# Kernel optimization log

Measured on AMD Instinct MI355X. Metric: run time of the kernel, lower is better.

The kernel has to match this reference:

```python
import jax, jax.numpy as jnp
import numpy as np

N_NODES = 65536
N_EDGES = 524288
N_GRAPHS = 512
G_NODES = 10000
NUM_DISEASES = 2000
IN_DIM = 128
HID = 256  # 2 * IN_DIM (z_emb concat feat)
D_FEAT = 512
C_FEAT = 512
MAX_Z = 4000


def setup_inputs() -> dict:
    key = jax.random.key(0)
    ks = jax.random.split(key, 20)
    rn = lambda k, shape: jax.random.normal(k, shape, dtype=jnp.float32) * 0.05
    return {
        "z": jax.random.randint(ks[0], (N_NODES,), 0, MAX_Z),
        "node_id": jnp.sort(jax.random.randint(ks[1], (N_NODES,), 0, G_NODES)),
        "src": jax.random.randint(ks[2], (N_EDGES,), 0, N_NODES),
        "dst": jax.random.randint(ks[3], (N_EDGES,), 0, N_NODES),
        "graph_ids": jnp.sort(jax.random.randint(ks[4], (N_NODES,), 0, N_GRAPHS)),
        "z_table": rn(ks[5], (MAX_Z, IN_DIM)),
        "d_feat_tab": rn(ks[6], (G_NODES, D_FEAT)),
        "c_feat_tab": rn(ks[7], (G_NODES, C_FEAT)),
        "Wd": rn(ks[8], (D_FEAT, IN_DIM)),
        "Wc": rn(ks[9], (C_FEAT, IN_DIM)),
        "gin_W1": rn(ks[10], (HID, HID)), "gin_b1": jnp.zeros((HID,), jnp.float32),
        "gin_W2": rn(ks[11], (HID, HID)), "gin_b2": jnp.zeros((HID,), jnp.float32),
        "sage_Wself": rn(ks[12], (HID, HID)),
        "sage_Wneigh": rn(ks[13], (HID, HID)),
        "sage_b": jnp.zeros((HID,), jnp.float32),
        "lin1_W": rn(ks[14], (HID, HID)), "lin1_b": jnp.zeros((HID,), jnp.float32),
        "lin2_W": rn(ks[15], (HID, 1)), "lin2_b": jnp.zeros((1,), jnp.float32),
    }


def reference(z, node_id, src, dst, graph_ids, z_table, d_feat_tab, c_feat_tab,
              Wd, Wc, gin_W1, gin_b1, gin_W2, gin_b2,
              sage_Wself, sage_Wneigh, sage_b, lin1_W, lin1_b, lin2_W, lin2_b):
    # --- input feature construction (Model.forward) ---
    z_emb = z_table[z]                               # [N, IN_DIM]
    d_proj = d_feat_tab[node_id] @ Wd                # d_fc (bias=False)
    c_proj = c_feat_tab[node_id] @ Wc                # c_fc (bias=False)
    disease = (node_id <= NUM_DISEASES)[:, None]
    # node_id is sorted -> masked concat order == node order
    feat = jnp.where(disease, d_proj, c_proj)        # [N, IN_DIM]
    x = jnp.concatenate([z_emb, feat], axis=1)       # [N, HID]
    # --- GINConv: sum aggregation, eps=0, mlp = Lin->ReLU->Lin ---
    agg = jax.ops.segment_sum(x[src], dst, num_segments=N_NODES)
    h = x + agg
    h = jax.nn.relu(h @ gin_W1 + gin_b1) @ gin_W2 + gin_b2
    # --- SAGEConv('mean'): fc_self(h) + fc_neigh(mean_neighbors) + bias ---
    deg = jax.ops.segment_sum(jnp.ones((N_EDGES,), h.dtype), dst, num_segments=N_NODES)
    mean_n = jax.ops.segment_sum(h[src], dst, num_segments=N_NODES) / jnp.maximum(deg, 1.0)[:, None]
    h = h @ sage_Wself + mean_n @ sage_Wneigh + sage_b
    # --- per-graph max pooling readout ---
    g = jax.ops.segment_max(h, graph_ids, num_segments=N_GRAPHS, indices_are_sorted=True)
    g = jnp.where(jnp.isfinite(g), g, 0.0)           # guard empty graphs
    # --- head: Linear -> ReLU -> (dropout p=0, eval) -> Linear ---
    h = jax.nn.relu(g @ lin1_W + lin1_b)
    return h @ lin2_W + lin2_b                       # [N_GRAPHS, 1]
```

## Files before the change

kernel.cpp:

```cpp
#include <hip/hip_runtime.h>
#include <hip/hip_bf16.h>

#define N_NODES     65536
#define N_EDGES     524288
#define N_GRAPHS    512
#define G_NODES_N   10000
#define NUM_DIS     2000
#define IN_DIM      128
#define HID         256
#define D_FEAT      512
#define MAX_Z       4000

typedef _Float16 half8 __attribute__((ext_vector_type(8)));
typedef float    f32x4 __attribute__((ext_vector_type(4)));

typedef __attribute__((address_space(1))) const void as1_void;
typedef __attribute__((address_space(3))) void       as3_void;

__global__ __launch_bounds__(256) void prep_kernel(
    const float* __restrict__ Ws, const float* __restrict__ Wn,
    const float* __restrict__ Wd, const float* __restrict__ Wc,
    const float* __restrict__ W1, const float* __restrict__ W2,
    const float* __restrict__ z_table,
    const int* __restrict__ z, const int* __restrict__ node_id,
    _Float16* __restrict__ WsT, _Float16* __restrict__ WnT,
    _Float16* __restrict__ WdT, _Float16* __restrict__ WcT,
    _Float16* __restrict__ W12P, _Float16* __restrict__ zt16,
    int2* __restrict__ zn2, int* __restrict__ cnt, int* __restrict__ flags)
{
    const int b = blockIdx.x;
    const int tid = threadIdx.x;
    if (b < 64) {
        __shared__ float tile[64][65];
        const float* W; _Float16* T; int K, N, k0, n0;
        if (b < 32) {
            const int mat = b >> 4, t = b & 15;
            K = HID; N = HID; k0 = (t >> 2) * 64; n0 = (t & 3) * 64;
            W = (mat == 0) ? Ws : Wn;
            T = (mat == 0) ? WsT : WnT;
        } else {
            const int bb = b - 32;
            const int mat = bb >> 4, t = bb & 15;
            K = D_FEAT; N = IN_DIM; k0 = (t >> 1) * 64; n0 = (t & 1) * 64;
            W = (mat == 0) ? Wd : Wc;
            T = (mat == 0) ? WdT : WcT;
        }
        const int tx = tid & 63, ty = tid >> 6;
        #pragma unroll
        for (int r = 0; r < 64; r += 4)
            tile[r + ty][tx] = W[(size_t)(k0 + r + ty) * N + n0 + tx];
        __syncthreads();
        #pragma unroll
        for (int c = 0; c < 64; c += 4)
            T[(size_t)(n0 + c + ty) * K + k0 + tx] = (_Float16)tile[tx][c + ty];
    } else if (b < 576) {
        const int bb = b - 64;
        const int mat = bb >> 8;
        const int k = bb & 255;
        const int n = tid;
        const float* W = mat ? W2 : W1;
        const float v = W[(size_t)k * HID + n];
        const size_t idx = (size_t)(mat * 8 + (k >> 5)) * 8192
                         + (size_t)((((k >> 3) & 3) * 256 + n) * 8 + (k & 7));
        W12P[idx] = (_Float16)v;
    } else if (b < 826) {
        const size_t base = ((size_t)(b - 576) * 256 + tid) * 8;
        const float4 f0 = *(const float4*)(z_table + base);
        const float4 f1 = *(const float4*)(z_table + base + 4);
        half8 h;
        h[0]=(_Float16)f0.x; h[1]=(_Float16)f0.y; h[2]=(_Float16)f0.z; h[3]=(_Float16)f0.w;
        h[4]=(_Float16)f1.x; h[5]=(_Float16)f1.y; h[6]=(_Float16)f1.z; h[7]=(_Float16)f1.w;
        *(half8*)(zt16 + base) = h;
    } else if (b < 890) {
        const int base = (b - 826) * 1024 + tid * 4;
        *(int4*)(cnt + base) = make_int4(0, 0, 0, 0);
        if (b == 826 && tid < 128) flags[tid] = 0;
    } else {
        const int i = (b - 890) * 256 + tid;
        zn2[i] = make_int2(z[i] << 8, node_id[i] << 8);
    }
}

__global__ __launch_bounds__(256) void proj_hist_kernel(
    const float* __restrict__ dtab, const float* __restrict__ ctab,
    const _Float16* __restrict__ WdT, const _Float16* __restrict__ WcT,
    _Float16* __restrict__ proj,
    const int* __restrict__ dst, int* __restrict__ cnt)
{
    const int blk = blockIdx.x;
    if (blk >= 79) {
        const int e = (blk - 79) * 256 + threadIdx.x;
        if (e < N_EDGES) atomicAdd(&cnt[dst[e]], 1);
        return;
    }
    __shared__ _Float16 Alds[128 * 40];
    __shared__ _Float16 Blds[128 * 40];
    const float* tab; const _Float16* WT; int base, M, bm;
    if (blk < 16) { tab = dtab; WT = WdT; base = 0;           M = NUM_DIS + 1;             bm = blk * 128; }
    else          { tab = ctab; WT = WcT; base = NUM_DIS + 1; M = G_NODES_N - NUM_DIS - 1; bm = (blk - 16) * 128; }
    const int tid  = threadIdx.x;
    const int wave = tid >> 6, lane = tid & 63;
    const int q    = lane >> 4, l16 = lane & 15;
    const int mbase = (wave & 1) * 64, nbase = (wave >> 1) * 64;
    const int r = tid >> 1, s = tid & 1;

    f32x4 acc[4][4] = {};

    for (int kc = 0; kc < 16; ++kc) {
        const int k0 = kc * 32;
        const int arow = min(bm + r, M - 1);
        const float* gA = tab + (size_t)(base + arow) * D_FEAT + k0 + s * 16;
        const _Float16* gB = WT + (size_t)r * D_FEAT + k0 + s * 16;
        const float4 f0 = ((const float4*)gA)[0];
        const float4 f1 = ((const float4*)gA)[1];
        const float4 f2 = ((const float4*)gA)[2];
        const float4 f3 = ((const float4*)gA)[3];
        const half8 hb0 = *(const half8*)gB;
        const half8 hb1 = *(const half8*)(gB + 8);
        half8 h0, h1;
        h0[0]=(_Float16)f0.x; h0[1]=(_Float16)f0.y; h0[2]=(_Float16)f0.z; h0[3]=(_Float16)f0.w;
        h0[4]=(_Float16)f1.x; h0[5]=(_Float16)f1.y; h0[6]=(_Float16)f1.z; h0[7]=(_Float16)f1.w;
        h1[0]=(_Float16)f2.x; h1[1]=(_Float16)f2.y; h1[2]=(_Float16)f2.z; h1[3]=(_Float16)f2.w;
        h1[4]=(_Float16)f3.x; h1[5]=(_Float16)f3.y; h1[6]=(_Float16)f3.z; h1[7]=(_Float16)f3.w;
        __syncthreads();
        *(half8*)&Alds[r * 40 + s * 16]     = h0;
        *(half8*)&Alds[r * 40 + s * 16 + 8] = h1;
        *(half8*)&Blds[r * 40 + s * 16]     = hb0;
        *(half8*)&Blds[r * 40 + s * 16 + 8] = hb1;
        __syncthreads();
        half8 a[4], b[4];
        #pragma unroll
        for (int i = 0; i < 4; ++i)
            a[i] = *(const half8*)&Alds[(mbase + i * 16 + l16) * 40 + q * 8];
        #pragma unroll
        for (int j = 0; j < 4; ++j)
            b[j] = *(const half8*)&Blds[(nbase + j * 16 + l16) * 40 + q * 8];
        #pragma unroll
        for (int i = 0; i < 4; ++i)
            #pragma unroll
            for (int j = 0; j < 4; ++j)
                acc[i][j] = __builtin_amdgcn_mfma_f32_16x16x32_f16(a[i], b[j], acc[i][j], 0, 0, 0);
    }

    #pragma unroll
    for (int j = 0; j < 4; ++j) {
        const int colg = nbase + j * 16 + l16;
        #pragma unroll
        for (int i = 0; i < 4; ++i) {
            #pragma unroll
            for (int rr = 0; rr < 4; ++rr) {
                const int row = bm + mbase + i * 16 + q * 4 + rr;
                if (row < M)
                    proj[(size_t)(base + row) * IN_DIM + colg] = (_Float16)acc[i][j][rr];
            }
        }
    }
}

__global__ __launch_bounds__(256) void scan_fused_kernel(
    const int* __restrict__ cnt, int* __restrict__ row_ptr,
    int* __restrict__ fill, int* __restrict__ flags,
    const int2* __restrict__ zn2, int2* __restrict__ pzn,
    int2* __restrict__ prbe, int* __restrict__ pnode,
    int* __restrict__ bhist)
{
    __shared__ int a[256], b[256];
    __shared__ int sums[64];
    __shared__ int segbase;
    __shared__ int hist[64];
    __shared__ int pos[64];
    const int t = threadIdx.x;
    const int blk = blockIdx.x;
    const int base = blk * 1024 + t * 4;
    const int4 c = *(const int4*)(cnt + base);
    const int s = c.x + c.y + c.z + c.w;
    a[t] = s;
    if (t < 64) hist[t] = 0;
    __syncthreads();
    int* in = a; int* out = b;
    for (int off = 1; off < 256; off <<= 1) {
        out[t] = in[t] + ((t >= off) ? in[t - off] : 0);
        __syncthreads();
        int* tmp = in; in = out; out = tmp;
    }
    if (t == 0) {
        atomicExch(&flags[64 + blk], in[255]);
        __threadfence();
        atomicAdd(&flags[0], 1);
        while (atomicAdd(&flags[0], 0) < 64) {}
    }
    __syncthreads();
    if (t < 64) sums[t] = atomicAdd(&flags[64 + t], 0);
    __syncthreads();
    if (t == 0) {
        int pfx = 0;
        for (int i = 0; i < blk; ++i) pfx += sums[i];
        segbase = pfx;
        if (blk == 63) {
            int tot = pfx;
            for (int i = blk; i < 64; ++i) tot += sums[i];
            row_ptr[N_NODES] = tot;
        }
    }
    __syncthreads();
    const int run = in[t] - s + segbase;
    int4 r;
    r.x = run; r.y = run + c.x; r.z = r.y + c.y; r.w = r.z + c.z;
    *(int4*)(row_ptr + base) = r;
    *(int4*)(fill + base) = r;

    const int bk0 = min(c.x, 63), bk1 = min(c.y, 63);
    const int bk2 = min(c.z, 63), bk3 = min(c.w, 63);
    atomicAdd(&hist[bk0], 1); atomicAdd(&hist[bk1], 1);
    atomicAdd(&hist[bk2], 1); atomicAdd(&hist[bk3], 1);
    __syncthreads();
    if (t < 64) bhist[blk * 64 + t] = hist[t];
    __threadfence();
    if (t == 0) {
        atomicAdd(&flags[1], 1);
        while (atomicAdd(&flags[1], 0) < 64) {}
    }
    __syncthreads();
    if (t < 64) {
        int pre = 0, tot = 0;
        for (int i = 0; i < 64; ++i) {
            const int v = atomicAdd(&bhist[i * 64 + t], 0);
            if (i < blk) pre += v;
            tot += v;
        }
        hist[t] = tot;
        pos[t] = pre;
    }
    __syncthreads();
    if (t == 0) {
        int run2 = 0;
        for (int i = 0; i < 64; ++i) { const int tt = hist[i]; hist[i] = run2; run2 += tt; }
    }
    __syncthreads();
    if (t < 64) pos[t] = hist[t] + pos[t];
    __syncthreads();
    const int begs[4] = { r.x, r.y, r.z, r.w };
    const int ends[4] = { r.y, r.z, r.w, r.w + c.w };
    const int bks[4]  = { bk0, bk1, bk2, bk3 };
    #pragma unroll
    for (int k = 0; k < 4; ++k) {
        const int p = atomicAdd(&pos[bks[k]], 1);
        pzn[p]   = zn2[base + k];
        prbe[p]  = make_int2(begs[k], ends[k]);
        pnode[p] = base + k;
    }
}

__global__ __launch_bounds__(256) void scatter_kernel(
    const int* __restrict__ src, const int* __restrict__ dst,
    const int2* __restrict__ zn2,
    int* __restrict__ fill, int* __restrict__ col, int2* __restrict__ colzn)
{
    const int e = blockIdx.x * 256 + threadIdx.x;
    if (e < N_EDGES) {
        const int s = src[e];
        const int pos = atomicAdd(&fill[dst[e]], 1);
        col[pos] = s << 9;
        colzn[pos] = zn2[s];
    }
}

__global__ __launch_bounds__(256, 6) void gather_kernel(
    const int2* __restrict__ prbe, const int2* __restrict__ pzn,
    const int2* __restrict__ colzn,
    const _Float16* __restrict__ zt16, const _Float16* __restrict__ proj,
    _Float16* __restrict__ AGG)
{
    const int i = blockIdx.x * 16 + (threadIdx.x >> 4);
    const int l = threadIdx.x & 15;
    const bool isz = (l < 8);
    const char* tab = isz ? (const char*)zt16 : (const char*)proj;
    const int loff = (l & 7) * 32;
    const int2 be = prbe[i];
    const int2 zn = pzn[i];
    float acc[16];
    {
        const half8* sp = (const half8*)(tab + (isz ? zn.x : zn.y) + loff);
        const half8 v0 = sp[0], v1 = sp[1];
        #pragma unroll
        for (int k = 0; k < 8; ++k) { acc[k] = (float)v0[k]; acc[8 + k] = (float)v1[k]; }
    }
    int e = be.x;
    const int end = be.y;
    int2 iA, iB, iC, iD;
    if (e + 4 <= end) {
        iA = colzn[e]; iB = colzn[e + 1]; iC = colzn[e + 2]; iD = colzn[e + 3];
    }
    for (; e + 4 <= end; e += 4) {
        const half8* sA = (const half8*)(tab + (isz ? iA.x : iA.y) + loff);
        const half8* sB = (const half8*)(tab + (isz ? iB.x : iB.y) + loff);
        const half8* sC = (const half8*)(tab + (isz ? iC.x : iC.y) + loff);
        const half8* sD = (const half8*)(tab + (isz ? iD.x : iD.y) + loff);
        const half8 a0 = sA[0], a1 = sA[1];
        const half8 b0 = sB[0], b1 = sB[1];
        const half8 c0 = sC[0], c1 = sC[1];
        const half8 d0 = sD[0], d1 = sD[1];
        if (e + 8 <= end) {
            iA = colzn[e + 4]; iB = colzn[e + 5];
            iC = colzn[e + 6]; iD = colzn[e + 7];
        }
        #pragma unroll
        for (int k = 0; k < 8; ++k) {
            acc[k]     += ((float)a0[k] + (float)b0[k]) + ((float)c0[k] + (float)d0[k]);
            acc[8 + k] += ((float)a1[k] + (float)b1[k]) + ((float)c1[k] + (float)d1[k]);
        }
    }
    for (; e < end; ++e) {
        const int2 j = colzn[e];
        const half8* s = (const half8*)(tab + (isz ? j.x : j.y) + loff);
        const half8 v0 = s[0], v1 = s[1];
        #pragma unroll
        for (int k = 0; k < 8; ++k) { acc[k] += (float)v0[k]; acc[8 + k] += (float)v1[k]; }
    }
    half8 o0, o1;
    #pragma unroll
    for (int k = 0; k < 8; ++k) { o0[k] = (_Float16)acc[k]; o1[k] = (_Float16)acc[8 + k]; }
    _Float16* dst = AGG + (size_t)i * 256 + l * 16;
    *(half8*)dst = o0;
    *(half8*)(dst + 8) = o1;
}

__global__ __launch_bounds__(256) void gin_mlp_kernel(
    const _Float16* __restrict__ AGG, const int* __restrict__ pnode,
    const _Float16* __restrict__ W12P,
    const float* __restrict__ b1, const float* __restrict__ b2,
    _Float16* __restrict__ H)
{
    __shared__ _Float16 Apanel[64 * 264];
    __shared__ _Float16 Blds[8192];
    __shared__ int prows[64];

    const int bm   = blockIdx.x * 64;
    const int tid  = threadIdx.x;
    const int wave = tid >> 6, lane = tid & 63;
    const int q    = lane >> 4, l16 = lane & 15;
    const int nbase = wave * 64;
    const int sb   = wave * 256 + lane;

    if (tid < 64) prows[tid] = pnode[bm + tid];

    #pragma unroll
    for (int tt = 0; tt < 4; ++tt) {
        const int seg = (wave * 4 + tt) * 64 + lane;
        __builtin_amdgcn_global_load_lds((as1_void*)(W12P + seg * 8),
            (as3_void*)&Blds[(wave * 4 + tt) * 64 * 8], 16, 0, 0);
    }

    {
        const int ar = tid >> 2, acs = (tid & 3) * 64;
        const _Float16* asrc = AGG + (size_t)(bm + ar) * 256 + acs;
        half8 av[8];
        #pragma unroll
        for (int k = 0; k < 8; ++k) av[k] = *(const half8*)(asrc + k * 8);
        #pragma unroll
        for (int k = 0; k < 8; ++k)
            *(half8*)&Apanel[ar * 264 + acs + k * 8] = av[k];
    }
    __syncthreads();

    half8 pf0, pf1, pf2, pf3;
    auto pfetch = [&](int c) {
        const _Float16* s = W12P + (size_t)c * 8192 + (size_t)sb * 8;
        pf0 = *(const half8*)(s);
        pf1 = *(const half8*)(s + 512);
        pf2 = *(const half8*)(s + 1024);
        pf3 = *(const half8*)(s + 1536);
    };
    pfetch(1);

    f32x4 acc[4][4] = {};
    for (int c = 0; c < 16; ++c) {
        const int kl = (c & 7) * 32;
        half8 a[4], b[4];
        #pragma unroll
        for (int i = 0; i < 4; ++i)
            a[i] = *(const half8*)&Apanel[(i * 16 + l16) * 264 + kl + q * 8];
        #pragma unroll
        for (int j = 0; j < 4; ++j)
            b[j] = *(const half8*)&Blds[(q * 256 + nbase + j * 16 + l16) * 8];
        #pragma unroll
        for (int i = 0; i < 4; ++i)
            #pragma unroll
            for (int j = 0; j < 4; ++j)
                acc[i][j] = __builtin_amdgcn_mfma_f32_16x16x32_f16(a[i], b[j], acc[i][j], 0, 0, 0);
        if (c == 15) break;
        __syncthreads();
        *(half8*)&Blds[sb * 8]         = pf0;
        *(half8*)&Blds[(sb + 64) * 8]  = pf1;
        *(half8*)&Blds[(sb + 128) * 8] = pf2;
        *(half8*)&Blds[(sb + 192) * 8] = pf3;
        if (c == 7) {
            #pragma unroll
            for (int j = 0; j < 4; ++j) {
                const int colg = nbase + j * 16 + l16;
                const float bv = b1[colg];
                #pragma unroll
                for (int i = 0; i < 4; ++i)
                    #pragma unroll
                    for (int rr = 0; rr < 4; ++rr) {
                        const float v = fmaxf(acc[i][j][rr] + bv, 0.0f);
                        Apanel[(i * 16 + q * 4 + rr) * 264 + colg] = (_Float16)v;
                        acc[i][j][rr] = 0.0f;
                    }
            }
        }
        if (c < 14) pfetch(c + 2);
        __syncthreads();
    }

    #pragma unroll
    for (int j = 0; j < 4; ++j) {
        const int colg = nbase + j * 16 + l16;
        const float bv = b2[colg];
        #pragma unroll
        for (int i = 0; i < 4; ++i)
            #pragma unroll
            for (int rr = 0; rr < 4; ++rr) {
                const int rowl = i * 16 + q * 4 + rr;
                H[(size_t)prows[rowl] * HID + colg] = (_Float16)(acc[i][j][rr] + bv);
            }
    }
}

__global__ __launch_bounds__(256) void csr_agg_kernel(
    const int2* __restrict__ prbe, const int* __restrict__ pnode,
    const int* __restrict__ col,
    const _Float16* __restrict__ F, _Float16* __restrict__ OUT)
{
    const int t = threadIdx.x;
    const int q = t & 31;
    const int pr = t >> 5;
    const int ia = blockIdx.x * 16 + pr * 2;
    const int ib = ia + 1;
    const int2 beA = prbe[ia];
    const int2 beB = prbe[ib];
    int eA = beA.x, eB = beB.x;
    const int endA = beA.y, endB = beB.y;
    const char* Fb = (const char*)F + q * 16;
    float accA[8] = {0.f,0.f,0.f,0.f,0.f,0.f,0.f,0.f};
    float accB[8] = {0.f,0.f,0.f,0.f,0.f,0.f,0.f,0.f};

    int cA0, cA1, cA2, cA3, cB0, cB1, cB2, cB3;
    bool mA = (eA + 4 <= endA), mB = (eB + 4 <= endB);
    if (mA) { cA0 = col[eA]; cA1 = col[eA+1]; cA2 = col[eA+2]; cA3 = col[eA+3]; }
    if (mB) { cB0 = col[eB]; cB1 = col[eB+1]; cB2 = col[eB+2]; cB3 = col[eB+3]; }

    while (mA && mB) {
        const half8 a0 = *(const half8*)(Fb + cA0);
        const half8 a1 = *(const half8*)(Fb + cA1);
        const half8 a2 = *(const half8*)(Fb + cA2);
        const half8 a3 = *(const half8*)(Fb + cA3);
        const half8 b0 = *(const half8*)(Fb + cB0);
        const half8 b1 = *(const half8*)(Fb + cB1);
        const half8 b2 = *(const half8*)(Fb + cB2);
        const half8 b3 = *(const half8*)(Fb + cB3);
        eA += 4; eB += 4;
        mA = (eA + 4 <= endA); mB = (eB + 4 <= endB);
        if (mA) { cA0 = col[eA]; cA1 = col[eA+1]; cA2 = col[eA+2]; cA3 = col[eA+3]; }
        if (mB) { cB0 = col[eB]; cB1 = col[eB+1]; cB2 = col[eB+2]; cB3 = col[eB+3]; }
        #pragma unroll
        for (int k = 0; k < 8; ++k) {
            accA[k] += ((float)a0[k] + (float)a1[k]) + ((float)a2[k] + (float)a3[k]);
            accB[k] += ((float)b0[k] + (float)b1[k]) + ((float)b2[k] + (float)b3[k]);
        }
    }
    while (mA) {
        const half8 a0 = *(const half8*)(Fb + cA0);
        const half8 a1 = *(const half8*)(Fb + cA1);
        const half8 a2 = *(const half8*)(Fb + cA2);
        const half8 a3 = *(const half8*)(Fb + cA3);
        eA += 4;
        mA = (eA + 4 <= endA);
        if (mA) { cA0 = col[eA]; cA1 = col[eA+1]; cA2 = col[eA+2]; cA3 = col[eA+3]; }
        #pragma unroll
        for (int k = 0; k < 8; ++k)
            accA[k] += ((float)a0[k] + (float)a1[k]) + ((float)a2[k] + (float)a3[k]);
    }
    while (mB) {
        const half8 b0 = *(const half8*)(Fb + cB0);
        const half8 b1 = *(const half8*)(Fb + cB1);
        const half8 b2 = *(const half8*)(Fb + cB2);
        const half8 b3 = *(const half8*)(Fb + cB3);
        eB += 4;
        mB = (eB + 4 <= endB);
        if (mB) { cB0 = col[eB]; cB1 = col[eB+1]; cB2 = col[eB+2]; cB3 = col[eB+3]; }
        #pragma unroll
        for (int k = 0; k < 8; ++k)
            accB[k] += ((float)b0[k] + (float)b1[k]) + ((float)b2[k] + (float)b3[k]);
    }
    for (; eA < endA; ++eA) {
        const half8 v = *(const half8*)(Fb + col[eA]);
        #pragma unroll
        for (int k = 0; k < 8; ++k) accA[k] += (float)v[k];
    }
    for (; eB < endB; ++eB) {
        const half8 v = *(const half8*)(Fb + col[eB]);
        #pragma unroll
        for (int k = 0; k < 8; ++k) accB[k] += (float)v[k];
    }

    const float rsA = 1.0f / fmaxf((float)(endA - beA.x), 1.0f);
    const float rsB = 1.0f / fmaxf((float)(endB - beB.x), 1.0f);
    half8 oA, oB;
    #pragma unroll
    for (int k = 0; k < 8; ++k) {
        oA[k] = (_Float16)(accA[k] * rsA);
        oB[k] = (_Float16)(accB[k] * rsB);
    }
    *(half8*)(OUT + (size_t)pnode[ia] * HID + q * 8) = oA;
    *(half8*)(OUT + (size_t)pnode[ib] * HID + q * 8) = oB;
}

__global__ __launch_bounds__(256) void mfma_gemm_kernel(
    const _Float16* __restrict__ A1, const _Float16* __restrict__ A2,
    const _Float16* __restrict__ B1T, const _Float16* __restrict__ B2T,
    const float* __restrict__ bias, _Float16* __restrict__ Ch)
{
    __shared__ _Float16 Alds[128 * 32];
    __shared__ _Float16 Blds[128 * 32];
    const int bm   = blockIdx.x * 128;
    const int bn   = blockIdx.y * 128;
    const int tid  = threadIdx.x;
    const int wave = tid >> 6, lane = tid & 63;
    const int q    = lane >> 4, l16 = lane & 15;
    const int mbase = (wave & 1) * 64, nbase = (wave >> 1) * 64;

    const int i0 = wave * 128 + lane;
    const int i1 = i0 + 64;
    const int r0 = i0 >> 2, s0 = i0 & 3;
    const int r1 = i1 >> 2, s1 = i1 & 3;

    half8 pa0, pa1, pb0, pb1;
    auto pfetch = [&](int kc) {
        const int k0 = (kc & 7) * 32;
        const _Float16* Ab = (kc < 8) ? A1 : A2;
        const _Float16* Bb = (kc < 8) ? B1T : B2T;
        pa0 = *(const half8*)(Ab + (size_t)(bm + r0) * HID + k0 + s0 * 8);
        pa1 = *(const half8*)(Ab + (size_t)(bm + r1) * HID + k0 + s1 * 8);
        pb0 = *(const half8*)(Bb + (size_t)(bn + r0) * HID + k0 + s0 * 8);
        pb1 = *(const half8*)(Bb + (size_t)(bn + r1) * HID + k0 + s1 * 8);
    };
    pfetch(0);

    f32x4 acc[4][4] = {};

    for (int kc = 0; kc < 16; ++kc) {
        __syncthreads();
        *(half8*)&Alds[i0 * 8] = pa0;
        *(half8*)&Alds[i1 * 8] = pa1;
        *(half8*)&Blds[i0 * 8] = pb0;
        *(half8*)&Blds[i1 * 8] = pb1;
        if (kc < 15) pfetch(kc + 1);
        __syncthreads();
        half8 a[4], b[4];
        #pragma unroll
        for (int i = 0; i < 4; ++i)
            a[i] = *(const half8*)&Alds[(mbase + i * 16 + l16) * 32 + q * 8];
        #pragma unroll
        for (int j = 0; j < 4; ++j)
            b[j] = *(const half8*)&Blds[(nbase + j * 16 + l16) * 32 + q * 8];
        #pragma unroll
        for (int i = 0; i < 4; ++i)
            #pragma unroll
            for (int j = 0; j < 4; ++j)
                acc[i][j] = __builtin_amdgcn_mfma_f32_16x16x32_f16(a[i], b[j], acc[i][j], 0, 0, 0);
    }

    #pragma unroll
    for (int j = 0; j < 4; ++j) {
        const int colg = bn + nbase + j * 16 + l16;
        const float bv = bias[colg];
        #pragma unroll
        for (int i = 0; i < 4; ++i) {
            #pragma unroll
            for (int rr = 0; rr < 4; ++rr) {
                const int rowg = bm + mbase + i * 16 + q * 4 + rr;
                Ch[(size_t)rowg * HID + colg] = (_Float16)(acc[i][j][rr] + bv);
            }
        }
    }
}

__global__ __launch_bounds__(256) void pool_head_kernel(
    const _Float16* __restrict__ H2, const int* __restrict__ gid,
    const float* __restrict__ W1, const float* __restrict__ b1,
    const float* __restrict__ W2, const float* __restrict__ b2,
    float* __restrict__ out)
{
    const int g = blockIdx.x;
    const int tid = threadIdx.x;
    int lo = 0, hi = N_NODES;
    while (lo < hi) { const int mid = (lo + hi) >> 1; if (gid[mid] < g) lo = mid + 1; else hi = mid; }
    const int start = lo;
    hi = N_NODES;
    while (lo < hi) { const int mid = (lo + hi) >> 1; if (gid[mid] < g + 1) lo = mid + 1; else hi = mid; }
    const int end = lo;

    const int rowofs = tid >> 5;
    const int q = tid & 31;
    float m8[8];
    #pragma unroll
    for (int k = 0; k < 8; ++k) m8[k] = -INFINITY;
    for (int i = start + rowofs; i < end; i += 8) {
        const half8 v = *(const half8*)(H2 + (size_t)i * HID + q * 8);
        #pragma unroll
        for (int k = 0; k < 8; ++k) m8[k] = fmaxf(m8[k], (float)v[k]);
    }
    __shared__ float part[8][256];
    #pragma unroll
    for (int k = 0; k < 8; ++k) part[rowofs][q * 8 + k] = m8[k];
    __syncthreads();
    __shared__ float row[HID];
    __shared__ float red[HID];
    const int j = tid;
    float m = part[0][j];
    #pragma unroll
    for (int r = 1; r < 8; ++r) m = fmaxf(m, part[r][j]);
    row[j] = (m == -INFINITY) ? 0.0f : m;
    __syncthreads();
    float acc = b1[j];
    #pragma unroll 8
    for (int k = 0; k < HID; ++k)
        acc = fmaf(row[k], W1[k * HID + j], acc);
    acc = fmaxf(acc, 0.f);
    red[j] = acc * W2[j];
    __syncthreads();
    for (int s = 128; s > 0; s >>= 1) {
        if (j < s) red[j] += red[j + s];
        __syncthreads();
    }
    if (j == 0) out[g] = red[0] + b2[0];
}

extern "C" void kernel_launch(void* const* d_in, const int* in_sizes, int n_in,
                              void* d_out, int out_size, void* d_ws, size_t ws_size,
                              hipStream_t stream)
{
    const int*   z         = (const int*)d_in[0];
    const int*   node_id   = (const int*)d_in[1];
    const int*   src       = (const int*)d_in[2];
    const int*   dst       = (const int*)d_in[3];
    const int*   graph_ids = (const int*)d_in[4];
    const float* z_table   = (const float*)d_in[5];
    const float* d_feat    = (const float*)d_in[6];
    const float* c_feat    = (const float*)d_in[7];
    const float* Wd        = (const float*)d_in[8];
    const float* Wc        = (const float*)d_in[9];
    const float* gin_W1    = (const float*)d_in[10];
    const float* gin_b1    = (const float*)d_in[11];
    const float* gin_W2    = (const float*)d_in[12];
    const float* gin_b2    = (const float*)d_in[13];
    const float* sage_Wself  = (const float*)d_in[14];
    const float* sage_Wneigh = (const float*)d_in[15];
    const float* sage_b    = (const float*)d_in[16];
    const float* lin1_W    = (const float*)d_in[17];
    const float* lin1_b    = (const float*)d_in[18];
    const float* lin2_W    = (const float*)d_in[19];
    const float* lin2_b    = (const float*)d_in[20];
    float* out = (float*)d_out;

    const size_t NH = (size_t)N_NODES * HID;
    char* wsb = (char*)d_ws;
    _Float16* Hh   = (_Float16*)wsb;                     wsb += NH * 2;
    _Float16* AGGh = (_Float16*)wsb;                     wsb += NH * 2;
    _Float16* H2h  = (_Float16*)wsb;                     wsb += NH * 2;
    _Float16* AGGx = (_Float16*)wsb;                     wsb += NH * 2;
    _Float16* projh= (_Float16*)wsb;                     wsb += (size_t)G_NODES_N * IN_DIM * 2;
    _Float16* W12P = (_Float16*)wsb;                     wsb += 16 * 8192 * 2;
    _Float16* WsT  = (_Float16*)wsb;                     wsb += HID * HID * 2;
    _Float16* WnT  = (_Float16*)wsb;                     wsb += HID * HID * 2;
    _Float16* WdT  = (_Float16*)wsb;                     wsb += D_FEAT * IN_DIM * 2;
    _Float16* WcT  = (_Float16*)wsb;                     wsb += D_FEAT * IN_DIM * 2;
    _Float16* zt16 = (_Float16*)wsb;                     wsb += (size_t)MAX_Z * IN_DIM * 2;
    int2* zn2      = (int2*)wsb;                         wsb += (size_t)N_NODES * 8;
    int2* colzn    = (int2*)wsb;                         wsb += (size_t)(N_EDGES + 8) * 8;
    int2* pzn      = (int2*)wsb;                         wsb += (size_t)N_NODES * 8;
    int2* prbe     = (int2*)wsb;                         wsb += (size_t)N_NODES * 8;
    int* pnode     = (int*)wsb;                          wsb += (size_t)N_NODES * 4;
    int* bhist     = (int*)wsb;                          wsb += 64 * 64 * 4;
    int* row_ptr   = (int*)wsb;                          wsb += (N_NODES + 4) * 4;
    int* cnt       = (int*)wsb;                          wsb += N_NODES * 4;
    int* fill      = (int*)wsb;                          wsb += N_NODES * 4;
    int* col       = (int*)wsb;                          wsb += N_EDGES * 4;
    int* flags     = (int*)wsb;                          wsb += 128 * 4;

    prep_kernel<<<1146, 256, 0, stream>>>(
        sage_Wself, sage_Wneigh, Wd, Wc, gin_W1, gin_W2, z_table, z, node_id,
        WsT, WnT, WdT, WcT, W12P, zt16, zn2, cnt, flags);

    proj_hist_kernel<<<79 + N_EDGES / 256, 256, 0, stream>>>(
        d_feat, c_feat, WdT, WcT, projh, dst, cnt);

    scan_fused_kernel<<<64, 256, 0, stream>>>(
        cnt, row_ptr, fill, flags, zn2, pzn, prbe, pnode, bhist);
    scatter_kernel<<<N_EDGES / 256, 256, 0, stream>>>(src, dst, zn2, fill, col, colzn);

    gather_kernel<<<N_NODES / 16, 256, 0, stream>>>(
        prbe, pzn, colzn, zt16, projh, AGGx);
    gin_mlp_kernel<<<N_NODES / 64, 256, 0, stream>>>(
        AGGx, pnode, W12P, gin_b1, gin_b2, Hh);

    csr_agg_kernel<<<N_NODES / 16, 256, 0, stream>>>(
        prbe, pnode, col, Hh, AGGh);

    dim3 ggrid(N_NODES / 128, HID / 128);
    mfma_gemm_kernel<<<ggrid, 256, 0, stream>>>(Hh, AGGh, WsT, WnT, sage_b, H2h);

    pool_head_kernel<<<N_GRAPHS, 256, 0, stream>>>(
        H2h, graph_ids, lin1_W, lin1_b, lin2_W, lin2_b, out);
}
```

Before: 356.7 us.

## Overlap self-GEMM with neighbor aggregation in one heterogeneous launch

The SAGE self-projection h@Wself now runs in extra blocks of the CSR aggregation kernel, writing an fp32 partial into a new workspace buffer. The second GEMM then does only the neighbor half (K=256) and starts its accumulators from that partial. The aim is to fill the memory-bound aggregation with compute work and halve the final GEMM's K loop. The cost is an extra 64 MB fp32 write plus read of the partial, and the GEMM blocks share the launch's LDS and register budget with the aggregation blocks.

```diff
diff --git a/kernel.cpp b/kernel.cpp
--- a/kernel.cpp
+++ b/kernel.cpp
@@ -427,15 +427,80 @@
     }
 }
 
-__global__ __launch_bounds__(256) void csr_agg_kernel(
+__global__ __launch_bounds__(256) void agg_wsgemm_kernel(
     const int2* __restrict__ prbe, const int* __restrict__ pnode,
     const int* __restrict__ col,
-    const _Float16* __restrict__ F, _Float16* __restrict__ OUT)
-{
+    const _Float16* __restrict__ F, _Float16* __restrict__ OUT,
+    const _Float16* __restrict__ WsT, const float* __restrict__ bias,
+    float* __restrict__ P)
+{
+    __shared__ _Float16 Alds[128 * 32];
+    __shared__ _Float16 Blds[128 * 32];
+    const int blk = blockIdx.x;
     const int t = threadIdx.x;
+
+    if (blk < 1024) {
+        const int bm   = (blk >> 1) * 128;
+        const int bn   = (blk & 1) * 128;
+        const int wave = t >> 6, lane = t & 63;
+        const int q    = lane >> 4, l16 = lane & 15;
+        const int mbase = (wave & 1) * 64, nbase = (wave >> 1) * 64;
+
+        const int i0 = wave * 128 + lane;
+        const int i1 = i0 + 64;
+        const int r0 = i0 >> 2, s0 = i0 & 3;
+        const int r1 = i1 >> 2, s1 = i1 & 3;
+
+        half8 pa0, pa1, pb0, pb1;
+        auto pfetch = [&](int kc) {
+            const int k0 = kc * 32;
+            pa0 = *(const half8*)(F + (size_t)(bm + r0) * HID + k0 + s0 * 8);
+            pa1 = *(const half8*)(F + (size_t)(bm + r1) * HID + k0 + s1 * 8);
+            pb0 = *(const half8*)(WsT + (size_t)(bn + r0) * HID + k0 + s0 * 8);
+            pb1 = *(const half8*)(WsT + (size_t)(bn + r1) * HID + k0 + s1 * 8);
+        };
+        pfetch(0);
+
+        f32x4 acc[4][4] = {};
+        for (int kc = 0; kc < 8; ++kc) {
+            __syncthreads();
+            *(half8*)&Alds[i0 * 8] = pa0;
+            *(half8*)&Alds[i1 * 8] = pa1;
+            *(half8*)&Blds[i0 * 8] = pb0;
+            *(half8*)&Blds[i1 * 8] = pb1;
+            if (kc < 7) pfetch(kc + 1);
+            __syncthreads();
+            half8 a[4], b[4];
+            #pragma unroll
+            for (int i = 0; i < 4; ++i)
+                a[i] = *(const half8*)&Alds[(mbase + i * 16 + l16) * 32 + q * 8];
+            #pragma unroll
+            for (int j = 0; j < 4; ++j)
+                b[j] = *(const half8*)&Blds[(nbase + j * 16 + l16) * 32 + q * 8];
+            #pragma unroll
+            for (int i = 0; i < 4; ++i)
+                #pragma unroll
+                for (int j = 0; j < 4; ++j)
+                    acc[i][j] = __builtin_amdgcn_mfma_f32_16x16x32_f16(a[i], b[j], acc[i][j], 0, 0, 0);
+        }
+        #pragma unroll
+        for (int j = 0; j < 4; ++j) {
+            const int colg = bn + nbase + j * 16 + l16;
+            const float bv = bias[colg];
+            #pragma unroll
+            for (int i = 0; i < 4; ++i)
+                #pragma unroll
+                for (int rr = 0; rr < 4; ++rr) {
+                    const int rowg = bm + mbase + i * 16 + q * 4 + rr;
+                    P[(size_t)rowg * HID + colg] = acc[i][j][rr] + bv;
+                }
+        }
+        return;
+    }
+
     const int q = t & 31;
     const int pr = t >> 5;
-    const int ia = blockIdx.x * 16 + pr * 2;
+    const int ia = (blk - 1024) * 16 + pr * 2;
     const int ib = ia + 1;
     const int2 beA = prbe[ia];
     const int2 beB = prbe[ib];
@@ -516,10 +581,9 @@
     *(half8*)(OUT + (size_t)pnode[ib] * HID + q * 8) = oB;
 }
 
-__global__ __launch_bounds__(256) void mfma_gemm_kernel(
-    const _Float16* __restrict__ A1, const _Float16* __restrict__ A2,
-    const _Float16* __restrict__ B1T, const _Float16* __restrict__ B2T,
-    const float* __restrict__ bias, _Float16* __restrict__ Ch)
+__global__ __launch_bounds__(256) void gemm2_kernel(
+    const _Float16* __restrict__ A, const _Float16* __restrict__ BT,
+    const float* __restrict__ P, _Float16* __restrict__ Ch)
 {
     __shared__ _Float16 Alds[128 * 32];
     __shared__ _Float16 Blds[128 * 32];
@@ -537,25 +601,34 @@
 
     half8 pa0, pa1, pb0, pb1;
     auto pfetch = [&](int kc) {
-        const int k0 = (kc & 7) * 32;
-        const _Float16* Ab = (kc < 8) ? A1 : A2;
-        const _Float16* Bb = (kc < 8) ? B1T : B2T;
-        pa0 = *(const half8*)(Ab + (size_t)(bm + r0) * HID + k0 + s0 * 8);
-        pa1 = *(const half8*)(Ab + (size_t)(bm + r1) * HID + k0 + s1 * 8);
-        pb0 = *(const half8*)(Bb + (size_t)(bn + r0) * HID + k0 + s0 * 8);
-        pb1 = *(const half8*)(Bb + (size_t)(bn + r1) * HID + k0 + s1 * 8);
+        const int k0 = kc * 32;
+        pa0 = *(const half8*)(A + (size_t)(bm + r0) * HID + k0 + s0 * 8);
+        pa1 = *(const half8*)(A + (size_t)(bm + r1) * HID + k0 + s1 * 8);
+        pb0 = *(const half8*)(BT + (size_t)(bn + r0) * HID + k0 + s0 * 8);
+        pb1 = *(const half8*)(BT + (size_t)(bn + r1) * HID + k0 + s1 * 8);
     };
     pfetch(0);
 
-    f32x4 acc[4][4] = {};
-
-    for (int kc = 0; kc < 16; ++kc) {
+    f32x4 acc[4][4];
+    #pragma unroll
+    for (int j = 0; j < 4; ++j) {
+        const int colg = bn + nbase + j * 16 + l16;
+        #pragma unroll
+        for (int i = 0; i < 4; ++i)
+            #pragma unroll
+            for (int rr = 0; rr < 4; ++rr) {
+                const int rowg = bm + mbase + i * 16 + q * 4 + rr;
+                acc[i][j][rr] = P[(size_t)rowg * HID + colg];
+            }
+    }
+
+    for (int kc = 0; kc < 8; ++kc) {
         __syncthreads();
         *(half8*)&Alds[i0 * 8] = pa0;
         *(half8*)&Alds[i1 * 8] = pa1;
         *(half8*)&Blds[i0 * 8] = pb0;
         *(half8*)&Blds[i1 * 8] = pb1;
-        if (kc < 15) pfetch(kc + 1);
+        if (kc < 7) pfetch(kc + 1);
         __syncthreads();
         half8 a[4], b[4];
         #pragma unroll
@@ -574,13 +647,12 @@
     #pragma unroll
     for (int j = 0; j < 4; ++j) {
         const int colg = bn + nbase + j * 16 + l16;
-        const float bv = bias[colg];
         #pragma unroll
         for (int i = 0; i < 4; ++i) {
             #pragma unroll
             for (int rr = 0; rr < 4; ++rr) {
                 const int rowg = bm + mbase + i * 16 + q * 4 + rr;
-                Ch[(size_t)rowg * HID + colg] = (_Float16)(acc[i][j][rr] + bv);
+                Ch[(size_t)rowg * HID + colg] = (_Float16)acc[i][j][rr];
             }
         }
     }
@@ -670,6 +742,7 @@
     _Float16* AGGh = (_Float16*)wsb;                     wsb += NH * 2;
     _Float16* H2h  = (_Float16*)wsb;                     wsb += NH * 2;
     _Float16* AGGx = (_Float16*)wsb;                     wsb += NH * 2;
+    float* Pf32    = (float*)wsb;                        wsb += NH * 4;
     _Float16* projh= (_Float16*)wsb;                     wsb += (size_t)G_NODES_N * IN_DIM * 2;
     _Float16* W12P = (_Float16*)wsb;                     wsb += 16 * 8192 * 2;
     _Float16* WsT  = (_Float16*)wsb;                     wsb += HID * HID * 2;
@@ -705,11 +778,11 @@
     gin_mlp_kernel<<<N_NODES / 64, 256, 0, stream>>>(
         AGGx, pnode, W12P, gin_b1, gin_b2, Hh);
 
-    csr_agg_kernel<<<N_NODES / 16, 256, 0, stream>>>(
-        prbe, pnode, col, Hh, AGGh);
+    agg_wsgemm_kernel<<<1024 + N_NODES / 16, 256, 0, stream>>>(
+        prbe, pnode, col, Hh, AGGh, WsT, sage_b, Pf32);
 
     dim3 ggrid(N_NODES / 128, HID / 128);
-    mfma_gemm_kernel<<<ggrid, 256, 0, stream>>>(Hh, AGGh, WsT, WnT, sage_b, H2h);
+    gemm2_kernel<<<ggrid, 256, 0, stream>>>(AGGh, WnT, Pf32, H2h);
 
     pool_head_kernel<<<N_GRAPHS, 256, 0, stream>>>(
         H2h, graph_ids, lin1_W, lin1_b, lin2_W, lin2_b, out);
```

New measurement: 388.1 us. 1.09x slower.
